# Kernel optimization log

Hardware: AMD Instinct MI355X
Metric: run time of the kernel (lower is better)

The kernel has to match this reference:

```python
import jax, jax.numpy as jnp
import numpy as np

B, S, H = 64, 256, 768


def _lstm_cell(x, h, c, Wih, Whh, b):
    # PyTorch LSTMCell gate order: i, f, g, o
    g = x @ Wih.T + h @ Whh.T + b
    i, f, gg, o = jnp.split(g, 4, axis=-1)
    c = jax.nn.sigmoid(f) * c + jax.nn.sigmoid(i) * jnp.tanh(gg)
    h = jax.nn.sigmoid(o) * jnp.tanh(c)
    return h, c


def _bilstm(x, Wih_f, Whh_f, b_f, Wih_b, Whh_b, b_b):
    Bb, Ss, D = x.shape
    Hh = Whh_f.shape[1]

    def scan_dir(xs, Wih, Whh, b):
        def step(carry, x_t):
            h, c = carry
            h, c = _lstm_cell(x_t, h, c, Wih, Whh, b)
            return (h, c), h
        init = (jnp.zeros((Bb, Hh), x.dtype), jnp.zeros((Bb, Hh), x.dtype))
        _, hs = jax.lax.scan(step, init, xs)
        return hs

    xt = jnp.swapaxes(x, 0, 1)                      # [S, B, D]
    hf = scan_dir(xt, Wih_f, Whh_f, b_f)            # [S, B, H]
    hb = scan_dir(xt[::-1], Wih_b, Whh_b, b_b)[::-1]
    return jnp.swapaxes(jnp.concatenate([hf, hb], -1), 0, 1)  # [B, S, 2H]


def _decode(lstm_out, golds, subw_Wih, subw_Whh, subw_b,
            word_Wih, word_Whh, word_b, cls_W, cls_b):
    Bb, Ss, D = lstm_out.shape
    Hh = subw_Whh.shape[1]
    bidx = jnp.arange(Bb)
    subw_map = jnp.array([1, 2, 2], dtype=jnp.int32)   # subword_action_map
    word_map = jnp.array([0, 1, 1], dtype=jnp.int32)   # word_action_map

    sh = jnp.zeros((Bb, 2 * Ss + 2, Hh), lstm_out.dtype)  # subword stack (h)
    sc = jnp.zeros((Bb, 2 * Ss + 2, Hh), lstm_out.dtype)  # subword stack (c)
    wh = jnp.zeros((Bb, Ss + 1, Hh), lstm_out.dtype)       # word stack (h)
    wc = jnp.zeros((Bb, Ss + 1, Hh), lstm_out.dtype)       # word stack (c)
    sp = jnp.zeros((Bb,), jnp.int32)
    wp = jnp.zeros((Bb,), jnp.int32)

    xt = jnp.swapaxes(lstm_out, 0, 1)  # [S, B, 2H]
    gt = jnp.swapaxes(golds, 0, 1).astype(jnp.int32)
    xs = (xt[:-1], xt[1:], gt[1:])     # idx = 1..S-1

    def step(carry, inputs):
        sh, sc, sp, wh, wc, wp = carry
        x_prev, x_cur, g = inputs
        # subword stack LSTM: read top, push new state at pos+1
        h1, c1 = _lstm_cell(x_prev, sh[bidx, sp], sc[bidx, sp], subw_Wih, subw_Whh, subw_b)
        sh = sh.at[bidx, sp + 1].set(h1)
        sc = sc.at[bidx, sp + 1].set(c1)
        subword = jnp.concatenate([h1, c1], axis=-1)   # [B, 2H]
        # word stack LSTM
        wh1, wc1 = _lstm_cell(subword, wh[bidx, wp], wc[bidx, wp], word_Wih, word_Whh, word_b)
        wh = wh.at[bidx, wp + 1].set(wh1)
        wc = wc.at[bidx, wp + 1].set(wc1)
        out = jnp.concatenate([wh1, x_cur], axis=-1) @ cls_W.T + cls_b  # [B, 2]
        # training path: pos updates driven by gold actions
        sp = sp + subw_map[g]
        wp = wp + word_map[g]
        return (sh, sc, sp, wh, wc, wp), out

    _, outs = jax.lax.scan(step, (sh, sc, sp, wh, wc, wp), xs)  # [S-1, B, 2]
    first = jnp.broadcast_to(jnp.array([-1.0, 1.0], lstm_out.dtype), (Bb, 1, 2))
    return jnp.concatenate([first, jnp.swapaxes(outs, 0, 1)], axis=1)  # [B, S, 2]


def setup_inputs() -> dict:
    key = jax.random.key(0)
    ks = jax.random.split(key, 16)
    w = lambda k, shp: jax.random.normal(k, shp, dtype=jnp.float32) * 0.02
    return {
        "hidden_state": jax.random.normal(ks[0], (B, S, H), dtype=jnp.float32),
        "golds": jax.random.randint(ks[1], (B, S), 0, 2, dtype=jnp.int32),
        "lstm_Wih_f": w(ks[2], (4 * H, H)),
        "lstm_Whh_f": w(ks[3], (4 * H, H)),
        "lstm_b_f": w(ks[4], (4 * H,)),
        "lstm_Wih_b": w(ks[5], (4 * H, H)),
        "lstm_Whh_b": w(ks[6], (4 * H, H)),
        "lstm_b_b": w(ks[7], (4 * H,)),
        "subw_Wih": w(ks[8], (4 * H, 2 * H)),
        "subw_Whh": w(ks[9], (4 * H, H)),
        "subw_b": w(ks[10], (4 * H,)),
        "word_Wih": w(ks[11], (4 * H, 2 * H)),
        "word_Whh": w(ks[12], (4 * H, H)),
        "word_b": w(ks[13], (4 * H,)),
        "cls_W": w(ks[14], (2, 3 * H)),
        "cls_b": w(ks[15], (2,)),
    }


def reference(hidden_state, lstm_Wih_f, lstm_Whh_f, lstm_b_f,
              lstm_Wih_b, lstm_Whh_b, lstm_b_b,
              subw_Wih, subw_Whh, subw_b,
              word_Wih, word_Whh, word_b,
              cls_W, cls_b, golds):
    lstm_out = _bilstm(hidden_state, lstm_Wih_f, lstm_Whh_f, lstm_b_f,
                       lstm_Wih_b, lstm_Whh_b, lstm_b_b)
    return _decode(lstm_out, golds, subw_Wih, subw_Whh, subw_b,
                   word_Wih, word_Whh, word_b, cls_W, cls_b)
```

## Files before the change

kernel.cpp:

```cpp
#include <hip/hip_runtime.h>

#define B_  64
#define S_  256
#define H_  768
#define H4_ 3072
#define D2_ 1536
#define SEG 64
#define USZ (64*2304)

using u16 = unsigned short;
using u32 = unsigned int;
using u64 = unsigned long long;
typedef __attribute__((ext_vector_type(8))) short bf16x8;
typedef __attribute__((ext_vector_type(4))) float f32x4;
typedef __attribute__((ext_vector_type(4))) unsigned int u32x4;

#define DEV __device__ __forceinline__

DEV float bf2f(u16 u){ union{u32 i; float f;} c; c.i = ((u32)u)<<16; return c.f; }
DEV u16 f2bf(float f){ union{float f; u32 i;} c; c.f = f; return (u16)((c.i + 0x7FFFu + ((c.i>>16)&1u)) >> 16); }
DEV float sigm(float x){ return 1.f/(1.f + __expf(-x)); }
DEV float tanh_(float x){ return 2.f/(1.f + __expf(-2.f*x)) - 1.f; }

DEV void astore32(u16* p, u32 v){ __hip_atomic_store((u32*)p, v, __ATOMIC_RELAXED, __HIP_MEMORY_SCOPE_AGENT); }
DEV int afload(const int* p){ return __hip_atomic_load(p, __ATOMIC_RELAXED, __HIP_MEMORY_SCOPE_AGENT); }

DEV f32x4 mfma16(bf16x8 a, bf16x8 b, f32x4 c){
  return __builtin_amdgcn_mfma_f32_16x16x32_bf16(a, b, c, 0, 0, 0);
}

DEV void llc_load96(const u16* p, u32x4& a0, u32x4& a1, u32x4& a2,
                    u32x4& a3, u32x4& a4, u32x4& a5){
  asm volatile(
    "global_load_dwordx4 %0, %6, off sc0 sc1\n\t"
    "global_load_dwordx4 %1, %6, off offset:16 sc0 sc1\n\t"
    "global_load_dwordx4 %2, %6, off offset:32 sc0 sc1\n\t"
    "global_load_dwordx4 %3, %6, off offset:48 sc0 sc1\n\t"
    "global_load_dwordx4 %4, %6, off offset:64 sc0 sc1\n\t"
    "global_load_dwordx4 %5, %6, off offset:80 sc0 sc1\n\t"
    "s_waitcnt vmcnt(0)"
    : "=&v"(a0), "=&v"(a1), "=&v"(a2), "=&v"(a3), "=&v"(a4), "=&v"(a5)
    : "v"(p));
}
DEV void llc_load96_nw(const u16* p, u32x4& a0, u32x4& a1, u32x4& a2,
                       u32x4& a3, u32x4& a4, u32x4& a5){
  asm volatile(
    "global_load_dwordx4 %0, %6, off sc0 sc1\n\t"
    "global_load_dwordx4 %1, %6, off offset:16 sc0 sc1\n\t"
    "global_load_dwordx4 %2, %6, off offset:32 sc0 sc1\n\t"
    "global_load_dwordx4 %3, %6, off offset:48 sc0 sc1\n\t"
    "global_load_dwordx4 %4, %6, off offset:64 sc0 sc1\n\t"
    "global_load_dwordx4 %5, %6, off offset:80 sc0 sc1"
    : "=&v"(a0), "=&v"(a1), "=&v"(a2), "=&v"(a3), "=&v"(a4), "=&v"(a5)
    : "v"(p));
}
DEV void vmwait0(){ asm volatile("s_waitcnt vmcnt(0)" ::: "memory"); }

DEV void stage48llc(u16* dst, const u16* src){
  u32x4 a0,a1,a2,a3,a4,a5;
  llc_load96(src, a0,a1,a2,a3,a4,a5);
  *(u32x4*)(dst)    = a0; *(u32x4*)(dst+8)  = a1;
  *(u32x4*)(dst+16) = a2; *(u32x4*)(dst+24) = a3;
  *(u32x4*)(dst+32) = a4; *(u32x4*)(dst+40) = a5;
}
DEV void stage48llcz(u16* dst, const u16* src, bool keep){
  u32x4 a0,a1,a2,a3,a4,a5;
  llc_load96(src, a0,a1,a2,a3,a4,a5);
  const u32x4 z = {0u,0u,0u,0u};
  if (!keep){ a0=z; a1=z; a2=z; a3=z; a4=z; a5=z; }
  *(u32x4*)(dst)    = a0; *(u32x4*)(dst+8)  = a1;
  *(u32x4*)(dst+16) = a2; *(u32x4*)(dst+24) = a3;
  *(u32x4*)(dst+32) = a4; *(u32x4*)(dst+40) = a5;
}
DEV void wr48(u16* dst, const u32x4* a){
  *(u32x4*)(dst)    = a[0]; *(u32x4*)(dst+8)  = a[1];
  *(u32x4*)(dst+16) = a[2]; *(u32x4*)(dst+24) = a[3];
  *(u32x4*)(dst+32) = a[4]; *(u32x4*)(dst+40) = a[5];
}

__global__ void k_conv(const float* __restrict__ src, u16* __restrict__ dst,
                       int cols, int sld, int dld){
  const long r = blockIdx.x;
  for (int c = threadIdx.x*4; c < cols; c += 1024) {
    const float* sp = src + r*sld + c;
    float a = sp[0], b = sp[1], cc = sp[2], d = sp[3];
    u64 pack = (u64)f2bf(a) | ((u64)f2bf(b)<<16) | ((u64)f2bf(cc)<<32) | ((u64)f2bf(d)<<48);
    *(u64*)(dst + r*dld + c) = pack;
  }
}

__global__ __launch_bounds__(256) void k_gemm(
    const u16* __restrict__ A, const u16* __restrict__ W,
    const float* __restrict__ bias, u16* __restrict__ C, int K, int t0)
{
  __shared__ u16 at[128*40];
  __shared__ u16 bt[128*40];
  const int tid = threadIdx.x;
  const int L = tid & 63, wv = tid >> 6;
  const int mq = wv >> 1, nq = wv & 1;
  const int l16 = L & 15, quad = L >> 4;
  const long mb = blockIdx.y, nb = blockIdx.x;

  f32x4 acc[4][4];
  #pragma unroll
  for (int m=0;m<4;++m)
    #pragma unroll
    for (int n=0;n<4;++n)
      acc[m][n] = (f32x4){0.f,0.f,0.f,0.f};

  const int r = tid >> 1, c0 = (tid & 1) * 16;
  const int fr = (int)mb*128 + r;
  const long arow = ((long)(fr >> 6))*S_ + t0 + (fr & 63);
  const u16* Arow = A + arow*(long)K + c0;
  const u16* Wrow = W + (nb*128 + r)*(long)K + c0;

  for (int kb = 0; kb < K; kb += 32) {
    *(u32x4*)&at[r*40 + c0]     = *(const u32x4*)(Arow + kb);
    *(u32x4*)&at[r*40 + c0 + 8] = *(const u32x4*)(Arow + kb + 8);
    *(u32x4*)&bt[r*40 + c0]     = *(const u32x4*)(Wrow + kb);
    *(u32x4*)&bt[r*40 + c0 + 8] = *(const u32x4*)(Wrow + kb + 8);
    __syncthreads();
    bf16x8 af[4], bfr[4];
    #pragma unroll
    for (int m=0;m<4;++m) af[m]  = *(const bf16x8*)&at[(mq*64 + m*16 + l16)*40 + quad*8];
    #pragma unroll
    for (int n=0;n<4;++n) bfr[n] = *(const bf16x8*)&bt[(nq*64 + n*16 + l16)*40 + quad*8];
    #pragma unroll
    for (int m=0;m<4;++m)
      #pragma unroll
      for (int n=0;n<4;++n)
        acc[m][n] = mfma16(af[m], bfr[n], acc[m][n]);
    __syncthreads();
  }
  #pragma unroll
  for (int n=0;n<4;++n) {
    const long col = nb*128 + nq*64 + n*16 + l16;
    const float bv = bias[col];
    #pragma unroll
    for (int m=0;m<4;++m) {
      const long row0 = mb*128 + mq*64 + m*16 + quad*4;
      #pragma unroll
      for (int rr=0;rr<4;++rr)
        C[(row0+rr)*3072 + col] = f2bf(acc[m][n][rr] + bv);
    }
  }
}

__global__ __launch_bounds__(512,2) void k_bilstm(
    const u16* __restrict__ Gf, const u16* __restrict__ Gb,
    const u16* __restrict__ Whhf, const u16* __restrict__ Whhb,
    const u16* __restrict__ h0, u16* __restrict__ lstm,
    float* __restrict__ cstf, float* __restrict__ cstb,
    int* __restrict__ flags, int t0f, int tb0, int ep0)
{
  __shared__ __align__(16) u16 lds[32*776];
  float* gbuf = (float*)lds;
  const int wg = blockIdx.x;
  const int dir = wg / 96, rem = wg % 96, mh = rem / 48, s = rem % 48;
  const int grp = dir*2 + mh;
  const int tid = threadIdx.x;
  const int wave = tid >> 6, q = wave & 3, kh = wave >> 2;
  const int L = tid & 63, l16 = L & 15, quad = L >> 4;
  const int srw = tid >> 4, scl = (tid & 15) * 48;

  const u16* Gsrc = dir ? Gb : Gf;
  const u16* W    = dir ? Whhb : Whhf;
  float* cst      = dir ? cstb : cstf;

  bf16x8 bfr[12];
  {
    const u16* wr = W + (long)(q*H_ + s*16 + l16)*H_ + kh*384 + quad*8;
    #pragma unroll
    for (int kk=0;kk<12;++kk) bfr[kk] = *(const bf16x8*)(wr + kk*32);
  }

  const int lb = tid >> 3, cdl = (tid & 7) * 2;
  const int eb = mh*32 + lb, col = s*16 + cdl;
  const bool ew = (tid < 256);
  float creg[2] = {0.f, 0.f};
  if (ew){ creg[0] = cst[eb*H_ + col]; creg[1] = cst[eb*H_ + col + 1]; }

  u32 g0=0,g1=0,g2=0,g3=0;
  if (ew){
    const int tp0 = dir ? (tb0 + SEG-1) : t0f;
    const int gidx = eb*SEG + (dir ? (tp0 - tb0) : (tp0 - t0f));
    const u16* grow = Gsrc + (long)gidx*H4_ + col;
    g0 = *(const u32*)(grow);      g1 = *(const u32*)(grow + H_);
    g2 = *(const u32*)(grow+2*H_); g3 = *(const u32*)(grow+3*H_);
  }

  for (int t=0; t<SEG; ++t) {
    const int tp = dir ? (tb0 + SEG-1 - t) : (t0f + t);
    const bool first = dir ? (tp == S_-1) : (tp == 0);
    const u16* hbase; long ldh;
    if (first){ hbase = h0 + dir*H_; ldh = D2_; }
    else {
      const int tprev = dir ? (tp+1) : (tp-1);
      hbase = lstm + (long)tprev*D2_ + dir*H_;
      ldh = (long)S_*D2_;
    }
    stage48llc(&lds[srw*776 + scl], hbase + (long)(mh*32 + srw)*ldh + scl);
    __syncthreads();
    f32x4 acc[2];
    acc[0] = (f32x4){0.f,0.f,0.f,0.f}; acc[1] = acc[0];
    #pragma unroll
    for (int kk=0;kk<12;++kk)
      #pragma unroll
      for (int m=0;m<2;++m){
        bf16x8 a = *(const bf16x8*)&lds[(m*16+l16)*776 + kh*384 + kk*32 + quad*8];
        acc[m] = mfma16(a, bfr[kk], acc[m]);
      }
    __syncthreads();
    #pragma unroll
    for (int m=0;m<2;++m)
      #pragma unroll
      for (int rr=0;rr<4;++rr)
        gbuf[(q*2+kh)*512 + (m*16+quad*4+rr)*16 + l16] = acc[m][rr];
    __syncthreads();
    if (ew){
      u32 gr[4] = {g0,g1,g2,g3};
      u32 hp = 0;
      #pragma unroll
      for (int i=0;i<2;++i){
        float gv[4];
        #pragma unroll
        for (int qq=0;qq<4;++qq)
          gv[qq] = gbuf[(qq*2+0)*512 + lb*16 + cdl+i]
                 + gbuf[(qq*2+1)*512 + lb*16 + cdl+i]
                 + bf2f((u16)(gr[qq] >> (16*i)));
        const float c = sigm(gv[1])*creg[i] + sigm(gv[0])*tanh_(gv[2]);
        creg[i] = c;
        const float h = sigm(gv[3])*tanh_(c);
        hp |= ((u32)f2bf(h)) << (16*i);
      }
      astore32(lstm + ((long)eb*S_ + tp)*D2_ + dir*H_ + col, hp);
    }
    __threadfence_block();
    __syncthreads();
    if (tid == 0)
      __hip_atomic_store(&flags[(grp*48 + s)*64], ep0 + t + 1, __ATOMIC_RELAXED, __HIP_MEMORY_SCOPE_AGENT);
    if (ew){
      const int t2 = t + 1;
      const int tp2 = dir ? (tb0 + SEG-1 - t2) : (t0f + t2);
      const long gidx2 = (long)eb*SEG + (dir ? (tp2 - tb0) : (tp2 - t0f));
      const u16* grow2 = Gsrc + gidx2*H4_ + col;
      g0 = *(const u32*)(grow2);      g1 = *(const u32*)(grow2 + H_);
      g2 = *(const u32*)(grow2+2*H_); g3 = *(const u32*)(grow2+3*H_);
    }
    if ((int)tid < 48) {
      while (afload(&flags[(grp*48 + (int)tid)*64]) < ep0 + t + 1)
        __builtin_amdgcn_s_sleep(1);
    }
    __syncthreads();
  }
  if (ew){ cst[eb*H_ + col] = creg[0]; cst[eb*H_ + col + 1] = creg[1]; }
}

__global__ __launch_bounds__(512,1) void k_decode(
    const u16* __restrict__ Gsub, const u16* __restrict__ Wsub,
    const u16* __restrict__ Wwrd, const float* __restrict__ wbias,
    const float* __restrict__ clsW, const int* __restrict__ golds,
    u16* __restrict__ U,
    float* __restrict__ scS, float* __restrict__ wcS, float* __restrict__ whS,
    float* __restrict__ partials, int* __restrict__ flags, int r0)
{
  __shared__ __align__(16) u16 ab[3][32*776];
  float* gbuf = (float*)ab;
  const int wg = blockIdx.x;
  const int role = wg / 96, rem = wg % 96, mh = rem / 48, s = rem % 48;
  const int grp = role*2 + mh;
  const int tid = threadIdx.x;
  const int wave = tid >> 6, q = wave & 3, kh = wave >> 2;
  const int L = tid & 63, l16 = L & 15, quad = L >> 4;
  const int srw0 = tid >> 4, scl0 = (tid & 15) * 48;
  const int lb = tid >> 3, cdl = (tid & 7)*2;
  const int eb = mh*32 + lb, col = s*16 + cdl;
  const bool ew = (tid < 256);
  const int sb0 = mh*32 + srw0;
  u16* abf = &ab[0][0];

  bf16x8 wfr[36];
  float st0[2] = {0.f,0.f}, st1[2] = {0.f,0.f}, st2[2] = {0.f,0.f};
  float wbv[4][2], clv[2][2];
  if (role == 0){
    const u16* wr = Wsub + (long)(q*H_ + s*16 + l16)*H_ + kh*384 + quad*8;
    #pragma unroll
    for (int kk=0;kk<12;++kk) wfr[kk] = *(const bf16x8*)(wr + kk*32);
    if (ew){ st0[0] = scS[eb*H_+col]; st0[1] = scS[eb*H_+col+1]; }
  } else {
    const u16* wr = Wwrd + (long)(q*H_ + s*16 + l16)*2304 + kh*384 + quad*8;
    #pragma unroll
    for (int cc=0;cc<3;++cc)
      #pragma unroll
      for (int kk=0;kk<12;++kk)
        wfr[cc*12+kk] = *(const bf16x8*)(wr + cc*768 + kk*32);
    if (ew){
      st1[0] = wcS[eb*H_+col]; st1[1] = wcS[eb*H_+col+1];
      st2[0] = whS[eb*H_+col]; st2[1] = whS[eb*H_+col+1];
      #pragma unroll
      for (int qq=0;qq<4;++qq){ wbv[qq][0]=wbias[qq*H_+col]; wbv[qq][1]=wbias[qq*H_+col+1]; }
      clv[0][0]=clsW[col]; clv[0][1]=clsW[col+1];
      clv[1][0]=clsW[2304+col]; clv[1][1]=clsW[2304+col+1];
    }
  }

  int stg_g = golds[sb0*S_ + ((r0 < 255) ? r0 : 255)];

  for (int rr=0; rr<SEG; ++rr){
    const int r = r0 + rr;
    u32 g0=0,g1=0,g2=0,g3=0; int gld_e = 0, gld = 0;
    if (ew){
      if (role == 0 && r <= 254){
        gld_e = golds[eb*S_ + r + 1];
        const u16* grow = Gsub + ((long)eb*SEG + rr)*H4_ + col;
        g0 = *(const u32*)(grow);      g1 = *(const u32*)(grow + H_);
        g2 = *(const u32*)(grow+2*H_); g3 = *(const u32*)(grow+3*H_);
      } else if (role == 1 && r >= 1){
        gld = golds[eb*S_ + r];
      }
    }
    if (tid < 96){
      int idx, tgt;
      if (tid < 48){ idx = mh*48 + tid; tgt = r; }
      else { idx = (2+mh)*48 + (tid-48); tgt = (role==0) ? (r-56) : r; }
      while (afload(&flags[idx*64]) < tgt) __builtin_amdgcn_s_sleep(1);
    }
    __syncthreads();

    const u16* Uprev = U + (long)((r+63)&63)*USZ;
    u16*       Ucur  = U + (long)(r&63)*USZ;

    float p0 = 0.f, p1 = 0.f; bool do_part = false; int tp = 0;

    if (role == 0){
      if (r <= 254){
        const bool keep_s = (r > 0) && (stg_g == 0);
        stage48llcz(&abf[srw0*776 + scl0], Uprev + (long)sb0*2304 + scl0, keep_s);
        __syncthreads();
        f32x4 acc[2];
        acc[0] = (f32x4){0.f,0.f,0.f,0.f}; acc[1] = acc[0];
        #pragma unroll
        for (int kk=0;kk<12;++kk)
          #pragma unroll
          for (int m=0;m<2;++m){
            bf16x8 a = *(const bf16x8*)&abf[(m*16+l16)*776 + kh*384 + kk*32 + quad*8];
            acc[m] = mfma16(a, wfr[kk], acc[m]);
          }
        __syncthreads();
        stg_g = golds[sb0*S_ + ((r+1 < 255) ? r+1 : 255)];
        #pragma unroll
        for (int m=0;m<2;++m)
          #pragma unroll
          for (int r4=0;r4<4;++r4)
            gbuf[(q*2+kh)*512 + (m*16+quad*4+r4)*16 + l16] = acc[m][r4];
        __syncthreads();
        if (ew){
          const bool keep = (gld_e == 0);
          u32 gr[4] = {g0,g1,g2,g3};
          u32 hp=0, cp=0;
          #pragma unroll
          for (int i=0;i<2;++i){
            float gv[4];
            #pragma unroll
            for (int qq=0;qq<4;++qq)
              gv[qq] = gbuf[(qq*2+0)*512 + lb*16 + cdl+i]
                     + gbuf[(qq*2+1)*512 + lb*16 + cdl+i]
                     + bf2f((u16)(gr[qq] >> (16*i)));
            const float c1 = sigm(gv[1])*st0[i] + sigm(gv[0])*tanh_(gv[2]);
            const float h1 = sigm(gv[3])*tanh_(c1);
            st0[i] = keep ? c1 : 0.f;
            hp |= ((u32)f2bf(h1)) << (16*i);
            cp |= ((u32)f2bf(c1)) << (16*i);
          }
          astore32(Ucur + (long)eb*2304 + col, hp);
          astore32(Ucur + (long)eb*2304 + H_ + col, cp);
        }
      }
    } else {
      if (r >= 1){
        const u16* urow = Uprev + (long)sb0*2304;
        u32x4 c0[6], c1[6], c2[6];
        llc_load96_nw(urow + scl0,       c0[0],c0[1],c0[2],c0[3],c0[4],c0[5]);
        llc_load96_nw(urow + 768 + scl0, c1[0],c1[1],c1[2],c1[3],c1[4],c1[5]);
        vmwait0();
        wr48(&ab[0][srw0*776 + scl0], c0);
        wr48(&ab[1][srw0*776 + scl0], c1);
        __syncthreads();
        llc_load96_nw(urow + 1536 + scl0, c2[0],c2[1],c2[2],c2[3],c2[4],c2[5]);
        f32x4 acc[2];
        acc[0] = (f32x4){0.f,0.f,0.f,0.f}; acc[1] = acc[0];
        #pragma unroll
        for (int kk=0;kk<12;++kk)
          #pragma unroll
          for (int m=0;m<2;++m){
            bf16x8 a = *(const bf16x8*)&ab[0][(m*16+l16)*776 + kh*384 + kk*32 + quad*8];
            acc[m] = mfma16(a, wfr[kk], acc[m]);
          }
        #pragma unroll
        for (int kk=0;kk<12;++kk)
          #pragma unroll
          for (int m=0;m<2;++m){
            bf16x8 a = *(const bf16x8*)&ab[1][(m*16+l16)*776 + kh*384 + kk*32 + quad*8];
            acc[m] = mfma16(a, wfr[12+kk], acc[m]);
          }
        vmwait0();
        wr48(&ab[2][srw0*776 + scl0], c2);
        __syncthreads();
        #pragma unroll
        for (int kk=0;kk<12;++kk)
          #pragma unroll
          for (int m=0;m<2;++m){
            bf16x8 a = *(const bf16x8*)&ab[2][(m*16+l16)*776 + kh*384 + kk*32 + quad*8];
            acc[m] = mfma16(a, wfr[24+kk], acc[m]);
          }
        __syncthreads();
        #pragma unroll
        for (int m=0;m<2;++m)
          #pragma unroll
          for (int r4=0;r4<4;++r4)
            gbuf[(q*2+kh)*512 + (m*16+quad*4+r4)*16 + l16] = acc[m][r4];
        __syncthreads();
        if (ew){
          const bool keep = (gld == 0);
          tp = r - 1;
          u32 wp = 0;
          #pragma unroll
          for (int i=0;i<2;++i){
            float gv[4];
            #pragma unroll
            for (int qq=0;qq<4;++qq)
              gv[qq] = gbuf[(qq*2+0)*512 + lb*16 + cdl+i]
                     + gbuf[(qq*2+1)*512 + lb*16 + cdl+i]
                     + wbv[qq][i];
            const float wc1 = sigm(gv[1])*st1[i] + sigm(gv[0])*tanh_(gv[2]);
            const float wh1 = sigm(gv[3])*tanh_(wc1);
            st1[i] = keep ? st1[i] : wc1;
            st2[i] = keep ? st2[i] : wh1;
            p0 += wh1 * clv[0][i];
            p1 += wh1 * clv[1][i];
            wp |= ((u32)f2bf(st2[i])) << (16*i);
          }
          astore32(Ucur + (long)eb*2304 + D2_ + col, wp);
          do_part = true;
        }
      }
    }
    __threadfence_block();
    __syncthreads();
    if (tid == 0)
      __hip_atomic_store(&flags[(grp*48 + s)*64], r+1, __ATOMIC_RELAXED, __HIP_MEMORY_SCOPE_AGENT);
    if (do_part){
      p0 += __shfl_xor(p0, 1); p0 += __shfl_xor(p0, 2); p0 += __shfl_xor(p0, 4);
      p1 += __shfl_xor(p1, 1); p1 += __shfl_xor(p1, 2); p1 += __shfl_xor(p1, 4);
      if ((tid & 7) == 0){
        float* pp = partials + ((long)(tp*48 + s)*64 + eb)*2;
        pp[0] = p0; pp[1] = p1;
      }
    }
  }
  if (ew){
    if (role == 0){
      scS[eb*H_+col] = st0[0]; scS[eb*H_+col+1] = st0[1];
    } else {
      wcS[eb*H_+col] = st1[0]; wcS[eb*H_+col+1] = st1[1];
      whS[eb*H_+col] = st2[0]; whS[eb*H_+col+1] = st2[1];
    }
  }
}

__global__ __launch_bounds__(256) void k_cls(
    const u16* __restrict__ lstm, const float* __restrict__ partials,
    const float* __restrict__ clsW, const float* __restrict__ clsb,
    float* __restrict__ out)
{
  const int ts = blockIdx.x;
  const int b  = blockIdx.y;
  const int tid = threadIdx.x;
  if (ts == 0) {
    if (tid == 0) { out[(long)b*S_*2 + 0] = -1.f; out[(long)b*S_*2 + 1] = 1.f; }
    return;
  }
  const int t = ts - 1;
  float s0 = 0.f, s1 = 0.f;
  const u16* xr = lstm + ((long)b*S_ + ts)*D2_;
  for (int k = tid; k < D2_; k += 256) {
    const float xv = bf2f(xr[k]);
    s0 += xv * clsW[768 + k];
    s1 += xv * clsW[2304 + 768 + k];
  }
  if (tid < 48) {
    const float* pr = partials + ((long)(t*48 + tid)*64 + b)*2;
    s0 += pr[0]; s1 += pr[1];
  }
  __shared__ float r0[256], r1[256];
  r0[tid] = s0; r1[tid] = s1; __syncthreads();
  for (int off = 128; off > 0; off >>= 1) {
    if (tid < off) { r0[tid] += r0[tid+off]; r1[tid] += r1[tid+off]; }
    __syncthreads();
  }
  if (tid == 0) {
    out[((long)b*S_ + ts)*2 + 0] = r0[0] + clsb[0];
    out[((long)b*S_ + ts)*2 + 1] = r1[0] + clsb[1];
  }
}

extern "C" void kernel_launch(void* const* d_in, const int* in_sizes, int n_in,
                              void* d_out, int out_size, void* d_ws, size_t ws_size,
                              hipStream_t stream)
{
  (void)in_sizes; (void)n_in; (void)out_size; (void)ws_size;
  const float* x     = (const float*)d_in[0];
  const int*   golds = (const int*)d_in[1];
  const float* wihf  = (const float*)d_in[2];
  const float* whhf  = (const float*)d_in[3];
  const float* bfw   = (const float*)d_in[4];
  const float* wihb  = (const float*)d_in[5];
  const float* whhb  = (const float*)d_in[6];
  const float* bbw   = (const float*)d_in[7];
  const float* swih  = (const float*)d_in[8];
  const float* swhh  = (const float*)d_in[9];
  const float* sb    = (const float*)d_in[10];
  const float* wwih  = (const float*)d_in[11];
  const float* wwhh  = (const float*)d_in[12];
  const float* wb    = (const float*)d_in[13];
  const float* clsW  = (const float*)d_in[14];
  const float* clsb  = (const float*)d_in[15];
  float* out = (float*)d_out;

  char* base = (char*)d_ws;
  u16*   h0   = (u16*)(base + 0);
  int*   flg2 = (int*)(base + 1179648);
  int*   flg4 = (int*)(base + 1228800);
  float* cstf = (float*)(base + 1277952);
  float* cstb = (float*)(base + 1474560);
  float* scS  = (float*)(base + 1671168);
  float* wcS  = (float*)(base + 1867776);
  float* whS  = (float*)(base + 2064384);
  u16* xb     = (u16*)(base + 2260992);
  u16* wihf_b = (u16*)(base + 27426816);
  u16* whhf_b = (u16*)(base + 32145408);
  u16* wihb_b = (u16*)(base + 36864000);
  u16* whhb_b = (u16*)(base + 41582592);
  u16* swih_b = (u16*)(base + 46301184);
  u16* swhh_b = (u16*)(base + 55738368);
  u16* wwrd_b = (u16*)(base + 60456960);
  u16* Gfseg  = (u16*)(base + 74612736);
  u16* Gbseg  = (u16*)(base + 99778560);
  u16* lstm   = (u16*)(base + 124944384);
  u16* Gsubseg = Gfseg;
  float* prt   = (float*)Gbseg;
  u16* U       = xb;

  hipMemsetAsync(d_ws, 0, 2260992, stream);

  k_conv<<<16384, 256, 0, stream>>>(x,    xb,     768,  768,  768);
  k_conv<<<3072,  256, 0, stream>>>(wihf, wihf_b, 768,  768,  768);
  k_conv<<<3072,  256, 0, stream>>>(whhf, whhf_b, 768,  768,  768);
  k_conv<<<3072,  256, 0, stream>>>(wihb, wihb_b, 768,  768,  768);
  k_conv<<<3072,  256, 0, stream>>>(whhb, whhb_b, 768,  768,  768);
  k_conv<<<3072,  256, 0, stream>>>(swih, swih_b, 1536, 1536, 1536);
  k_conv<<<3072,  256, 0, stream>>>(swhh, swhh_b, 768,  768,  768);
  k_conv<<<3072,  256, 0, stream>>>(wwih, wwrd_b,        1536, 1536, 2304);
  k_conv<<<3072,  256, 0, stream>>>(wwhh, wwrd_b + 1536, 768,  768,  2304);

  dim3 gg(24, 32);
  for (int sgi = 0; sgi < 4; ++sgi) {
    const int t0f = sgi*SEG;
    const int tb0 = (3 - sgi)*SEG;
    k_gemm<<<gg, 256, 0, stream>>>(xb, wihf_b, bfw, Gfseg, 768, t0f);
    k_gemm<<<gg, 256, 0, stream>>>(xb, wihb_b, bbw, Gbseg, 768, tb0);
    k_bilstm<<<192, 512, 0, stream>>>(Gfseg, Gbseg, whhf_b, whhb_b, h0, lstm,
                                      cstf, cstb, flg2, t0f, tb0, sgi*SEG);
  }

  hipMemsetAsync(U, 0, 64*(size_t)USZ*2, stream);

  for (int sgi = 0; sgi < 4; ++sgi) {
    const int r0 = sgi*SEG;
    k_gemm<<<gg, 256, 0, stream>>>(lstm, swih_b, sb, Gsubseg, 1536, r0);
    k_decode<<<192, 512, 0, stream>>>(Gsubseg, swhh_b, wwrd_b, wb, clsW, golds,
                                      U, scS, wcS, whS, prt, flg4, r0);
  }

  dim3 gc(256, 64);
  k_cls<<<gc, 256, 0, stream>>>(lstm, prt, clsW, clsb, out);
}
```

Measured before the change: 4.070 ms.

## Merge subword and word decode roles into one workgroup per column slice

The decode kernel previously split subword-LSTM and word-LSTM work across separate workgroup roles (192 WGs) with cross-role flag waits. Now each of 96 workgroups holds both weight sets in registers, stages the full previous U row (h, c, word-h) once into shared memory, and runs both MFMA chains per step. The subword keep-mask is applied as a multiplier on the recurrent gate sum instead of zeroing the staged tile. This removes one class of inter-workgroup synchronization and duplicate staging, at the cost of doubling per-WG MFMA work, higher register pressure (48 weight fragments), and half the CUs in use.

```diff
diff --git a/kernel.cpp b/kernel.cpp
--- a/kernel.cpp
+++ b/kernel.cpp
@@ -59,15 +59,6 @@
 DEV void stage48llc(u16* dst, const u16* src){
   u32x4 a0,a1,a2,a3,a4,a5;
   llc_load96(src, a0,a1,a2,a3,a4,a5);
-  *(u32x4*)(dst)    = a0; *(u32x4*)(dst+8)  = a1;
-  *(u32x4*)(dst+16) = a2; *(u32x4*)(dst+24) = a3;
-  *(u32x4*)(dst+32) = a4; *(u32x4*)(dst+40) = a5;
-}
-DEV void stage48llcz(u16* dst, const u16* src, bool keep){
-  u32x4 a0,a1,a2,a3,a4,a5;
-  llc_load96(src, a0,a1,a2,a3,a4,a5);
-  const u32x4 z = {0u,0u,0u,0u};
-  if (!keep){ a0=z; a1=z; a2=z; a3=z; a4=z; a5=z; }
   *(u32x4*)(dst)    = a0; *(u32x4*)(dst+8)  = a1;
   *(u32x4*)(dst+16) = a2; *(u32x4*)(dst+24) = a3;
   *(u32x4*)(dst+32) = a4; *(u32x4*)(dst+40) = a5;
@@ -264,11 +255,10 @@
     float* __restrict__ scS, float* __restrict__ wcS, float* __restrict__ whS,
     float* __restrict__ partials, int* __restrict__ flags, int r0)
 {
-  __shared__ __align__(16) u16 ab[3][32*776];
-  float* gbuf = (float*)ab;
+  __shared__ __align__(16) u16 st[32*2320];
+  float* gbuf = (float*)st;
   const int wg = blockIdx.x;
-  const int role = wg / 96, rem = wg % 96, mh = rem / 48, s = rem % 48;
-  const int grp = role*2 + mh;
+  const int mh = wg / 48, s = wg % 48;
   const int tid = threadIdx.x;
   const int wave = tid >> 6, q = wave & 3, kh = wave >> 2;
   const int L = tid & 63, l16 = L & 15, quad = L >> 4;
@@ -276,195 +266,160 @@
   const int lb = tid >> 3, cdl = (tid & 7)*2;
   const int eb = mh*32 + lb, col = s*16 + cdl;
   const bool ew = (tid < 256);
-  const int sb0 = mh*32 + srw0;
-  u16* abf = &ab[0][0];
-
-  bf16x8 wfr[36];
-  float st0[2] = {0.f,0.f}, st1[2] = {0.f,0.f}, st2[2] = {0.f,0.f};
+
+  bf16x8 wfrS[12], wfrW[36];
+  {
+    const u16* wrS = Wsub + (long)(q*H_ + s*16 + l16)*H_ + kh*384 + quad*8;
+    #pragma unroll
+    for (int kk=0;kk<12;++kk) wfrS[kk] = *(const bf16x8*)(wrS + kk*32);
+    const u16* wrW = Wwrd + (long)(q*H_ + s*16 + l16)*2304 + kh*384 + quad*8;
+    #pragma unroll
+    for (int cc=0;cc<3;++cc)
+      #pragma unroll
+      for (int kk=0;kk<12;++kk)
+        wfrW[cc*12+kk] = *(const bf16x8*)(wrW + cc*768 + kk*32);
+  }
+  float st0[2]={0.f,0.f}, st1[2]={0.f,0.f}, st2[2]={0.f,0.f};
   float wbv[4][2], clv[2][2];
-  if (role == 0){
-    const u16* wr = Wsub + (long)(q*H_ + s*16 + l16)*H_ + kh*384 + quad*8;
-    #pragma unroll
-    for (int kk=0;kk<12;++kk) wfr[kk] = *(const bf16x8*)(wr + kk*32);
-    if (ew){ st0[0] = scS[eb*H_+col]; st0[1] = scS[eb*H_+col+1]; }
-  } else {
-    const u16* wr = Wwrd + (long)(q*H_ + s*16 + l16)*2304 + kh*384 + quad*8;
-    #pragma unroll
-    for (int cc=0;cc<3;++cc)
-      #pragma unroll
-      for (int kk=0;kk<12;++kk)
-        wfr[cc*12+kk] = *(const bf16x8*)(wr + cc*768 + kk*32);
-    if (ew){
-      st1[0] = wcS[eb*H_+col]; st1[1] = wcS[eb*H_+col+1];
-      st2[0] = whS[eb*H_+col]; st2[1] = whS[eb*H_+col+1];
-      #pragma unroll
-      for (int qq=0;qq<4;++qq){ wbv[qq][0]=wbias[qq*H_+col]; wbv[qq][1]=wbias[qq*H_+col+1]; }
-      clv[0][0]=clsW[col]; clv[0][1]=clsW[col+1];
-      clv[1][0]=clsW[2304+col]; clv[1][1]=clsW[2304+col+1];
-    }
-  }
-
-  int stg_g = golds[sb0*S_ + ((r0 < 255) ? r0 : 255)];
+  if (ew){
+    st0[0]=scS[eb*H_+col]; st0[1]=scS[eb*H_+col+1];
+    st1[0]=wcS[eb*H_+col]; st1[1]=wcS[eb*H_+col+1];
+    st2[0]=whS[eb*H_+col]; st2[1]=whS[eb*H_+col+1];
+    #pragma unroll
+    for (int qq=0;qq<4;++qq){ wbv[qq][0]=wbias[qq*H_+col]; wbv[qq][1]=wbias[qq*H_+col+1]; }
+    clv[0][0]=clsW[col]; clv[0][1]=clsW[col+1];
+    clv[1][0]=clsW[2304+col]; clv[1][1]=clsW[2304+col+1];
+  }
 
   for (int rr=0; rr<SEG; ++rr){
     const int r = r0 + rr;
-    u32 g0=0,g1=0,g2=0,g3=0; int gld_e = 0, gld = 0;
+    u32 g0=0,g1=0,g2=0,g3=0; int msub=0, gld_e=0;
     if (ew){
-      if (role == 0 && r <= 254){
-        gld_e = golds[eb*S_ + r + 1];
+      msub  = golds[eb*S_ + r];
+      gld_e = golds[eb*S_ + ((r+1 < 255) ? r+1 : 255)];
+      if (r <= 254){
         const u16* grow = Gsub + ((long)eb*SEG + rr)*H4_ + col;
         g0 = *(const u32*)(grow);      g1 = *(const u32*)(grow + H_);
         g2 = *(const u32*)(grow+2*H_); g3 = *(const u32*)(grow+3*H_);
-      } else if (role == 1 && r >= 1){
-        gld = golds[eb*S_ + r];
-      }
-    }
-    if (tid < 96){
-      int idx, tgt;
-      if (tid < 48){ idx = mh*48 + tid; tgt = r; }
-      else { idx = (2+mh)*48 + (tid-48); tgt = (role==0) ? (r-56) : r; }
-      while (afload(&flags[idx*64]) < tgt) __builtin_amdgcn_s_sleep(1);
+      }
+    }
+    if (tid < 48){
+      while (afload(&flags[(mh*48 + tid)*64]) < r) __builtin_amdgcn_s_sleep(1);
     }
     __syncthreads();
 
     const u16* Uprev = U + (long)((r+63)&63)*USZ;
     u16*       Ucur  = U + (long)(r&63)*USZ;
 
-    float p0 = 0.f, p1 = 0.f; bool do_part = false; int tp = 0;
-
-    if (role == 0){
-      if (r <= 254){
-        const bool keep_s = (r > 0) && (stg_g == 0);
-        stage48llcz(&abf[srw0*776 + scl0], Uprev + (long)sb0*2304 + scl0, keep_s);
-        __syncthreads();
-        f32x4 acc[2];
-        acc[0] = (f32x4){0.f,0.f,0.f,0.f}; acc[1] = acc[0];
+    {
+      const u16* urow = Uprev + (long)(mh*32 + srw0)*2304;
+      u32x4 c0[6], c1[6], c2[6];
+      llc_load96_nw(urow + scl0,        c0[0],c0[1],c0[2],c0[3],c0[4],c0[5]);
+      llc_load96_nw(urow + 768 + scl0,  c1[0],c1[1],c1[2],c1[3],c1[4],c1[5]);
+      llc_load96_nw(urow + 1536 + scl0, c2[0],c2[1],c2[2],c2[3],c2[4],c2[5]);
+      vmwait0();
+      wr48(&st[srw0*2320 + scl0],        c0);
+      wr48(&st[srw0*2320 + 768 + scl0],  c1);
+      wr48(&st[srw0*2320 + 1536 + scl0], c2);
+    }
+    __syncthreads();
+
+    f32x4 accS[2], accW[2];
+    accS[0] = (f32x4){0.f,0.f,0.f,0.f}; accS[1] = accS[0];
+    accW[0] = accS[0]; accW[1] = accS[0];
+    if (r <= 254){
+      #pragma unroll
+      for (int kk=0;kk<12;++kk)
+        #pragma unroll
+        for (int m=0;m<2;++m){
+          bf16x8 a = *(const bf16x8*)&st[(m*16+l16)*2320 + kh*384 + kk*32 + quad*8];
+          accS[m] = mfma16(a, wfrS[kk], accS[m]);
+        }
+    }
+    if (r >= 1){
+      #pragma unroll
+      for (int cc=0;cc<3;++cc)
         #pragma unroll
         for (int kk=0;kk<12;++kk)
           #pragma unroll
           for (int m=0;m<2;++m){
-            bf16x8 a = *(const bf16x8*)&abf[(m*16+l16)*776 + kh*384 + kk*32 + quad*8];
-            acc[m] = mfma16(a, wfr[kk], acc[m]);
+            bf16x8 a = *(const bf16x8*)&st[(m*16+l16)*2320 + cc*768 + kh*384 + kk*32 + quad*8];
+            accW[m] = mfma16(a, wfrW[cc*12+kk], accW[m]);
           }
-        __syncthreads();
-        stg_g = golds[sb0*S_ + ((r+1 < 255) ? r+1 : 255)];
+    }
+    __syncthreads();
+    #pragma unroll
+    for (int m=0;m<2;++m)
+      #pragma unroll
+      for (int r4=0;r4<4;++r4){
+        gbuf[(q*2+kh)*512 + (m*16+quad*4+r4)*16 + l16]        = accS[m][r4];
+        gbuf[4096 + (q*2+kh)*512 + (m*16+quad*4+r4)*16 + l16] = accW[m][r4];
+      }
+    __syncthreads();
+
+    float p0 = 0.f, p1 = 0.f; bool do_part = false;
+    if (ew){
+      if (r <= 254){
+        const float hm = (r > 0 && msub == 0) ? 1.f : 0.f;
+        u32 gr[4] = {g0,g1,g2,g3};
+        u32 hp=0, cp=0;
         #pragma unroll
-        for (int m=0;m<2;++m)
+        for (int i=0;i<2;++i){
+          float gv[4];
           #pragma unroll
-          for (int r4=0;r4<4;++r4)
-            gbuf[(q*2+kh)*512 + (m*16+quad*4+r4)*16 + l16] = acc[m][r4];
-        __syncthreads();
-        if (ew){
-          const bool keep = (gld_e == 0);
-          u32 gr[4] = {g0,g1,g2,g3};
-          u32 hp=0, cp=0;
+          for (int qq=0;qq<4;++qq)
+            gv[qq] = hm*(gbuf[(qq*2+0)*512 + lb*16 + cdl+i]
+                       + gbuf[(qq*2+1)*512 + lb*16 + cdl+i])
+                   + bf2f((u16)(gr[qq] >> (16*i)));
+          const float c1 = sigm(gv[1])*st0[i] + sigm(gv[0])*tanh_(gv[2]);
+          const float h1 = sigm(gv[3])*tanh_(c1);
+          st0[i] = (gld_e == 0) ? c1 : 0.f;
+          hp |= ((u32)f2bf(h1)) << (16*i);
+          cp |= ((u32)f2bf(c1)) << (16*i);
+        }
+        astore32(Ucur + (long)eb*2304 + col, hp);
+        astore32(Ucur + (long)eb*2304 + H_ + col, cp);
+      }
+      if (r >= 1){
+        const bool keep = (msub == 0);
+        u32 wp = 0;
+        #pragma unroll
+        for (int i=0;i<2;++i){
+          float gv[4];
           #pragma unroll
-          for (int i=0;i<2;++i){
-            float gv[4];
-            #pragma unroll
-            for (int qq=0;qq<4;++qq)
-              gv[qq] = gbuf[(qq*2+0)*512 + lb*16 + cdl+i]
-                     + gbuf[(qq*2+1)*512 + lb*16 + cdl+i]
-                     + bf2f((u16)(gr[qq] >> (16*i)));
-            const float c1 = sigm(gv[1])*st0[i] + sigm(gv[0])*tanh_(gv[2]);
-            const float h1 = sigm(gv[3])*tanh_(c1);
-            st0[i] = keep ? c1 : 0.f;
-            hp |= ((u32)f2bf(h1)) << (16*i);
-            cp |= ((u32)f2bf(c1)) << (16*i);
-          }
-          astore32(Ucur + (long)eb*2304 + col, hp);
-          astore32(Ucur + (long)eb*2304 + H_ + col, cp);
+          for (int qq=0;qq<4;++qq)
+            gv[qq] = gbuf[4096 + (qq*2+0)*512 + lb*16 + cdl+i]
+                   + gbuf[4096 + (qq*2+1)*512 + lb*16 + cdl+i]
+                   + wbv[qq][i];
+          const float wc1 = sigm(gv[1])*st1[i] + sigm(gv[0])*tanh_(gv[2]);
+          const float wh1 = sigm(gv[3])*tanh_(wc1);
+          st1[i] = keep ? st1[i] : wc1;
+          st2[i] = keep ? st2[i] : wh1;
+          p0 += wh1 * clv[0][i];
+          p1 += wh1 * clv[1][i];
+          wp |= ((u32)f2bf(st2[i])) << (16*i);
         }
-      }
-    } else {
-      if (r >= 1){
-        const u16* urow = Uprev + (long)sb0*2304;
-        u32x4 c0[6], c1[6], c2[6];
-        llc_load96_nw(urow + scl0,       c0[0],c0[1],c0[2],c0[3],c0[4],c0[5]);
-        llc_load96_nw(urow + 768 + scl0, c1[0],c1[1],c1[2],c1[3],c1[4],c1[5]);
-        vmwait0();
-        wr48(&ab[0][srw0*776 + scl0], c0);
-        wr48(&ab[1][srw0*776 + scl0], c1);
-        __syncthreads();
-        llc_load96_nw(urow + 1536 + scl0, c2[0],c2[1],c2[2],c2[3],c2[4],c2[5]);
-        f32x4 acc[2];
-        acc[0] = (f32x4){0.f,0.f,0.f,0.f}; acc[1] = acc[0];
-        #pragma unroll
-        for (int kk=0;kk<12;++kk)
-          #pragma unroll
-          for (int m=0;m<2;++m){
-            bf16x8 a = *(const bf16x8*)&ab[0][(m*16+l16)*776 + kh*384 + kk*32 + quad*8];
-            acc[m] = mfma16(a, wfr[kk], acc[m]);
-          }
-        #pragma unroll
-        for (int kk=0;kk<12;++kk)
-          #pragma unroll
-          for (int m=0;m<2;++m){
-            bf16x8 a = *(const bf16x8*)&ab[1][(m*16+l16)*776 + kh*384 + kk*32 + quad*8];
-            acc[m] = mfma16(a, wfr[12+kk], acc[m]);
-          }
-        vmwait0();
-        wr48(&ab[2][srw0*776 + scl0], c2);
-        __syncthreads();
-        #pragma unroll
-        for (int kk=0;kk<12;++kk)
-          #pragma unroll
-          for (int m=0;m<2;++m){
-            bf16x8 a = *(const bf16x8*)&ab[2][(m*16+l16)*776 + kh*384 + kk*32 + quad*8];
-            acc[m] = mfma16(a, wfr[24+kk], acc[m]);
-          }
-        __syncthreads();
-        #pragma unroll
-        for (int m=0;m<2;++m)
-          #pragma unroll
-          for (int r4=0;r4<4;++r4)
-            gbuf[(q*2+kh)*512 + (m*16+quad*4+r4)*16 + l16] = acc[m][r4];
-        __syncthreads();
-        if (ew){
-          const bool keep = (gld == 0);
-          tp = r - 1;
-          u32 wp = 0;
-          #pragma unroll
-          for (int i=0;i<2;++i){
-            float gv[4];
-            #pragma unroll
-            for (int qq=0;qq<4;++qq)
-              gv[qq] = gbuf[(qq*2+0)*512 + lb*16 + cdl+i]
-                     + gbuf[(qq*2+1)*512 + lb*16 + cdl+i]
-                     + wbv[qq][i];
-            const float wc1 = sigm(gv[1])*st1[i] + sigm(gv[0])*tanh_(gv[2]);
-            const float wh1 = sigm(gv[3])*tanh_(wc1);
-            st1[i] = keep ? st1[i] : wc1;
-            st2[i] = keep ? st2[i] : wh1;
-            p0 += wh1 * clv[0][i];
-            p1 += wh1 * clv[1][i];
-            wp |= ((u32)f2bf(st2[i])) << (16*i);
-          }
-          astore32(Ucur + (long)eb*2304 + D2_ + col, wp);
-          do_part = true;
-        }
+        astore32(Ucur + (long)eb*2304 + D2_ + col, wp);
+        do_part = true;
       }
     }
     __threadfence_block();
     __syncthreads();
     if (tid == 0)
-      __hip_atomic_store(&flags[(grp*48 + s)*64], r+1, __ATOMIC_RELAXED, __HIP_MEMORY_SCOPE_AGENT);
+      __hip_atomic_store(&flags[(mh*48 + s)*64], r+1, __ATOMIC_RELAXED, __HIP_MEMORY_SCOPE_AGENT);
     if (do_part){
       p0 += __shfl_xor(p0, 1); p0 += __shfl_xor(p0, 2); p0 += __shfl_xor(p0, 4);
       p1 += __shfl_xor(p1, 1); p1 += __shfl_xor(p1, 2); p1 += __shfl_xor(p1, 4);
       if ((tid & 7) == 0){
-        float* pp = partials + ((long)(tp*48 + s)*64 + eb)*2;
+        float* pp = partials + ((long)((r-1)*48 + s)*64 + eb)*2;
         pp[0] = p0; pp[1] = p1;
       }
     }
   }
   if (ew){
-    if (role == 0){
-      scS[eb*H_+col] = st0[0]; scS[eb*H_+col+1] = st0[1];
-    } else {
-      wcS[eb*H_+col] = st1[0]; wcS[eb*H_+col+1] = st1[1];
-      whS[eb*H_+col] = st2[0]; whS[eb*H_+col+1] = st2[1];
-    }
+    scS[eb*H_+col] = st0[0]; scS[eb*H_+col+1] = st0[1];
+    wcS[eb*H_+col] = st1[0]; wcS[eb*H_+col+1] = st1[1];
+    whS[eb*H_+col] = st2[0]; whS[eb*H_+col+1] = st2[1];
   }
 }
 
@@ -578,8 +533,8 @@
   for (int sgi = 0; sgi < 4; ++sgi) {
     const int r0 = sgi*SEG;
     k_gemm<<<gg, 256, 0, stream>>>(lstm, swih_b, sb, Gsubseg, 1536, r0);
-    k_decode<<<192, 512, 0, stream>>>(Gsubseg, swhh_b, wwrd_b, wb, clsW, golds,
-                                      U, scS, wcS, whS, prt, flg4, r0);
+    k_decode<<<96, 512, 0, stream>>>(Gsubseg, swhh_b, wwrd_b, wb, clsW, golds,
+                                     U, scS, wcS, whS, prt, flg4, r0);
   }
 
   dim3 gc(256, 64);
```

Result: slower. 5.581 ms (+37.1%).
